# Optimization experiments

Measured on AMD Instinct MI355X. Metric: run time of the kernel, lower is better.

Reference implementation:

```python
import jax, jax.numpy as jnp
import numpy as np

B, S, D, H, MLP, RH, RANK, BS, E, RES = 64, 197, 768, 12, 3072, 512, 256, 2, 3, 1
EPS = 1e-5


def _ln(x, g, b):
    m = jnp.mean(x, -1, keepdims=True)
    v = jnp.mean((x - m) ** 2, -1, keepdims=True)
    return (x - m) / jnp.sqrt(v + EPS) * g + b


def setup_inputs() -> dict:
    key = jax.random.key(0)
    ks = jax.random.split(key, 16)
    n = lambda k, shp, s: (jax.random.normal(k, shp) * s).astype(jnp.float32)
    inp = {
        'x': n(ks[0], (B, S, D), 1.0),
        'LRA_mask': jnp.arange(2 ** BS, dtype=jnp.int32),
        'wq_w': n(ks[1], (D, D), 0.02), 'wq_b': jnp.zeros((D,), jnp.float32),
        'wk_w': n(ks[2], (D, D), 0.02), 'wk_b': jnp.zeros((D,), jnp.float32),
        'wv_w': n(ks[3], (D, D), 0.02), 'wv_b': jnp.zeros((D,), jnp.float32),
        'wo_w': n(ks[4], (D, D), 0.02), 'wo_b': jnp.zeros((D,), jnp.float32),
        'an_g': jnp.ones((D,), jnp.float32), 'an_b': jnp.zeros((D,), jnp.float32),
        'fc1_w': n(ks[5], (MLP, D), 0.02), 'fc1_b': jnp.zeros((MLP,), jnp.float32),
        'fc2_w': n(ks[6], (D, MLP), 0.02), 'fc2_b': jnp.zeros((D,), jnp.float32),
        'fn_g': jnp.ones((D,), jnp.float32), 'fn_b': jnp.zeros((D,), jnp.float32),
        'r1_w': n(ks[7], (RH, D), 0.01), 'r1_b': jnp.zeros((RH,), jnp.float32),
        'rn_g': jnp.ones((RH,), jnp.float32), 'rn_b': jnp.zeros((RH,), jnp.float32),
        'r2_w': n(ks[8], (BS * 2, RH), 0.01),
        'r2_b': jnp.array([0.1, 5.0] * BS, jnp.float32),
        'eA': n(ks[9], (E, RANK, D), 0.01),  # down_proj weights [out=rank, in=dim]
        'eB': n(ks[10], (E, D, RANK), 0.01),  # up_proj weights [out=dim, in=rank]
    }
    return inp


def reference(x, LRA_mask, wq_w, wq_b, wk_w, wk_b, wv_w, wv_b, wo_w, wo_b,
              an_g, an_b, fc1_w, fc1_b, fc2_w, fc2_b, fn_g, fn_b,
              r1_w, r1_b, rn_g, rn_b, r2_w, r2_b, eA, eB):
    hd = D // H
    # ---- RouterModule (eval mode: argmax hard routing) on block input ----
    rlog = jax.nn.silu(_ln(x @ r1_w.T + r1_b, rn_g, rn_b)) @ r2_w.T + r2_b
    rlog = rlog.reshape(B, S, BS, 2)
    bits = jnp.argmax(rlog, -1)               # [B,S,BS], value of channel-1 one-hot
    bits = bits.at[:, :RES, :].set(1)          # reserved tokens -> full-one key (identity)
    pw = 2 ** jnp.arange(BS - 1, -1, -1)
    idx = jnp.sum(bits * pw, -1)               # [B,S] routing key per token
    # ---- Attention (pre-norm) ----
    h = _ln(x, an_g, an_b)
    q = (h @ wq_w.T + wq_b).reshape(B, S, H, hd).transpose(0, 2, 1, 3)
    k = (h @ wk_w.T + wk_b).reshape(B, S, H, hd).transpose(0, 2, 1, 3)
    v = (h @ wv_w.T + wv_b).reshape(B, S, H, hd).transpose(0, 2, 1, 3)
    att = jax.nn.softmax(jnp.einsum('bhqd,bhkd->bhqk', q, k) / np.float32(np.sqrt(hd)), -1)
    o = jnp.einsum('bhqk,bhkd->bhqd', att, v).transpose(0, 2, 1, 3).reshape(B, S, D)
    x1 = x + (o @ wo_w.T + wo_b)
    # ---- FeedForward (pre-norm, exact GELU like torch nn.GELU) ----
    x2 = x1 + (jax.nn.gelu(_ln(x1, fn_g, fn_b) @ fc1_w.T + fc1_b, approximate=False) @ fc2_w.T + fc2_b)
    # ---- BlockPathApproximators: disjoint per-key residual LoRA experts ----
    # keys 0..E-1 have experts; key 2^BS-1 (full-one) is identity. LRA_mask covers all keys.
    down = jnp.einsum('bsd,erd->bser', x2, eA)            # [B,S,E,RANK]
    up = jnp.einsum('bser,edr->bsed', down, eB)           # [B,S,E,D]
    sel = (idx[..., None] == jnp.arange(E)).astype(x2.dtype)  # one-hot over experts [B,S,E]
    out = x2 + jnp.einsum('bsed,bse->bsd', up, sel)
    return out
```

## Files before the change

kernel.cpp:

```cpp
#include <hip/hip_runtime.h>
#include <cstdint>

#define B_SZ   64
#define SEQ    197
#define DIM    768
#define NHEAD  12
#define HDK    64
#define MLP_D  3072
#define RH_D   512
#define RANK_D 256
#define NEXP   3
#define TOK    (B_SZ*SEQ)

typedef unsigned short u16;
typedef __attribute__((ext_vector_type(8))) short s16x8;
typedef __attribute__((ext_vector_type(4))) float f32x4;

static __device__ __forceinline__ u16 f2bf(float f) {
  unsigned u = __builtin_bit_cast(unsigned, f);
  u = u + 0x7FFFu + ((u >> 16) & 1u);
  return (u16)(u >> 16);
}

static __device__ __forceinline__ f32x4 mfma16(s16x8 a, s16x8 b, f32x4 c) {
  return __builtin_amdgcn_mfma_f32_16x16x32_bf16(a, b, c, 0, 0, 0);
}

static __device__ __forceinline__ void gload16(const u16* g, u16* l) {
  __builtin_amdgcn_global_load_lds(
      (const __attribute__((address_space(1))) unsigned int*)(const void*)g,
      (__attribute__((address_space(3))) unsigned int*)(void*)l,
      16, 0, 0);
}

static __device__ __forceinline__ float gelu_fast(float v) {
  const float u2 = 2.f * v * (0.7978845608f + 0.0356774081f * v * v);
  return v / (1.f + __expf(-u2));
}

__global__ void cvt_bf16(const float* __restrict__ in, u16* __restrict__ out, long n) {
  long i = ((long)blockIdx.x * blockDim.x + threadIdx.x) * 4;
  const long stride = (long)gridDim.x * blockDim.x * 4;
  for (; i < n; i += stride) {
    float4 v = *(const float4*)(in + i);
    unsigned r0 = (unsigned)f2bf(v.x) | ((unsigned)f2bf(v.y) << 16);
    unsigned r1 = (unsigned)f2bf(v.z) | ((unsigned)f2bf(v.w) << 16);
    *(uint2*)(out + i) = make_uint2(r0, r1);
  }
}

__global__ void concat3(const float* __restrict__ a, const float* __restrict__ b,
                        const float* __restrict__ c, float* __restrict__ out) {
  int i = blockIdx.x * 256 + threadIdx.x;
  if (i < DIM) { out[i] = a[i]; out[DIM + i] = b[i]; out[2*DIM + i] = c[i]; }
}

__global__ __launch_bounds__(256) void ln_rows(
    const float* __restrict__ x, const float* __restrict__ g,
    const float* __restrict__ bb, u16* __restrict__ out, int M)
{
  const int row = blockIdx.x * 4 + (threadIdx.x >> 6);
  const int lane = threadIdx.x & 63;
  if (row >= M) return;
  const float* xr = x + (long)row * DIM;
  float4 v[3];
  float s = 0.f, s2 = 0.f;
#pragma unroll
  for (int c = 0; c < 3; ++c) {
    v[c] = *(const float4*)(xr + c*256 + lane*4);
    s  += v[c].x + v[c].y + v[c].z + v[c].w;
    s2 += v[c].x*v[c].x + v[c].y*v[c].y + v[c].z*v[c].z + v[c].w*v[c].w;
  }
#pragma unroll
  for (int o = 1; o < 64; o <<= 1) { s += __shfl_xor(s, o); s2 += __shfl_xor(s2, o); }
  const float mean = s * (1.f/DIM);
  const float var  = s2 * (1.f/DIM) - mean*mean;
  const float rstd = rsqrtf(fmaxf(var, 0.f) + 1e-5f);
#pragma unroll
  for (int c = 0; c < 3; ++c) {
    const int idx = c*256 + lane*4;
    float4 gg = *(const float4*)(g + idx);
    float4 be = *(const float4*)(bb + idx);
    float y0 = (v[c].x - mean)*rstd*gg.x + be.x;
    float y1 = (v[c].y - mean)*rstd*gg.y + be.y;
    float y2 = (v[c].z - mean)*rstd*gg.z + be.z;
    float y3 = (v[c].w - mean)*rstd*gg.w + be.w;
    unsigned r0 = (unsigned)f2bf(y0) | ((unsigned)f2bf(y1) << 16);
    unsigned r1 = (unsigned)f2bf(y2) | ((unsigned)f2bf(y3) << 16);
    *(uint2*)(out + (long)row*DIM + idx) = make_uint2(r0, r1);
  }
}

template<int ACT, bool HAS_RES, bool OUT_F32, bool OUT_BF16>
__global__ __launch_bounds__(256) void gemm_bt(
    const u16* __restrict__ A, const u16* __restrict__ Bm,
    const float* __restrict__ bias, const float* __restrict__ res,
    float* __restrict__ Cf, u16* __restrict__ Cb,
    int ldc, int M, int N, int K)
{
  __shared__ __align__(16) u16 lA[2][128*32];
  __shared__ __align__(16) u16 lB[2][128*32];
  const int tid  = threadIdx.x;
  const int lane = tid & 63;
  const int wave = tid >> 6;
  const int m0 = blockIdx.y * 128;
  const int n0 = blockIdx.x * 128;
  const int fr = lane & 15, fg = lane >> 4;
  const int wr = wave >> 1, wc = wave & 1;
  const int srow = tid >> 2;
  const int scol = (tid & 3) * 8;

  const int ra0 = (m0 + srow      < M) ? (m0 + srow)      : (M - 1);
  const int ra1 = (m0 + 64 + srow < M) ? (m0 + 64 + srow) : (M - 1);
  const u16* pa0 = A  + (long)ra0 * K + scol;
  const u16* pa1 = A  + (long)ra1 * K + scol;
  const u16* pb0 = Bm + (long)(n0 + srow) * K + scol;
  const u16* pb1 = Bm + (long)(n0 + 64 + srow) * K + scol;

  auto STAGE = [&](int buf, int kt) {
    gload16(pa0 + kt, &lA[buf][srow*32 + scol]);
    gload16(pa1 + kt, &lA[buf][(64 + srow)*32 + scol]);
    gload16(pb0 + kt, &lB[buf][srow*32 + scol]);
    gload16(pb1 + kt, &lB[buf][(64 + srow)*32 + scol]);
  };

  f32x4 acc[4][4] = {};

  STAGE(0, 0);
  __syncthreads();
  int cur = 0;
  const int nsteps = K >> 5;
  for (int t = 0; t < nsteps; ++t) {
    if (t + 1 < nsteps) STAGE(cur ^ 1, (t + 1) << 5);
    s16x8 af[4], bfr[4];
#pragma unroll
    for (int m = 0; m < 4; ++m) af[m]  = *(const s16x8*)&lA[cur][(wr*64 + m*16 + fr)*32 + fg*8];
#pragma unroll
    for (int n = 0; n < 4; ++n) bfr[n] = *(const s16x8*)&lB[cur][(wc*64 + n*16 + fr)*32 + fg*8];
#pragma unroll
    for (int m = 0; m < 4; ++m)
#pragma unroll
      for (int n = 0; n < 4; ++n)
        acc[m][n] = mfma16(af[m], bfr[n], acc[m][n]);
    __syncthreads();
    cur ^= 1;
  }

#pragma unroll
  for (int m = 0; m < 4; ++m) {
#pragma unroll
    for (int n = 0; n < 4; ++n) {
      const int col = n0 + wc*64 + n*16 + fr;
      const float bv = bias[col];
#pragma unroll
      for (int r = 0; r < 4; ++r) {
        const int row = m0 + wr*64 + m*16 + fg*4 + r;
        if (row < M) {
          float v = acc[m][n][r] + bv;
          if constexpr (ACT == 1) v = gelu_fast(v);
          if constexpr (HAS_RES) v += res[(long)row * N + col];
          if constexpr (OUT_F32) Cf[(long)row * ldc + col] = v;
          if constexpr (OUT_BF16) Cb[(long)row * ldc + col] = f2bf(v);
        }
      }
    }
  }
}

__global__ __launch_bounds__(256, 2) void attn(const u16* __restrict__ qkv, u16* __restrict__ o) {
  __shared__ __align__(16) u16 Vt[64][232];
  __shared__ __align__(16) u16 Pl[4][16][232];
  const int bh = blockIdx.x;
  const int b = bh / NHEAD, h = bh - b * NHEAD;
  const int tid = threadIdx.x, lane = tid & 63, wave = tid >> 6;
  const long rbase = (long)b * SEQ * 2304;

  for (int i = tid; i < 224*64; i += 256) {
    const int s = i >> 6, d = i & 63;
    u16 val = 0;
    if (s < SEQ) val = qkv[rbase + (long)s*2304 + 1536 + h*HDK + d];
    Vt[d][s] = val;
  }
  for (int i = lane; i < 16*24; i += 64) {
    Pl[wave][i / 24][208 + i % 24] = 0;
  }
  __syncthreads();

  const int fr = lane & 15, fg = lane >> 4;
  for (int qb = wave; qb < 13; qb += 4) {
    const int q0 = qb * 16;
    int qrow = q0 + fr; if (qrow > SEQ-1) qrow = SEQ-1;
    const u16* qp = qkv + rbase + (long)qrow*2304 + h*HDK;
    const s16x8 a0 = *(const s16x8*)(qp + fg*8);
    const s16x8 a1 = *(const s16x8*)(qp + 32 + fg*8);
    f32x4 sc[13];
    for (int kb = 0; kb < 13; ++kb) {
      int krow = kb*16 + fr; if (krow > SEQ-1) krow = SEQ-1;
      const u16* kp = qkv + rbase + (long)krow*2304 + DIM + h*HDK;
      const s16x8 b0 = *(const s16x8*)(kp + fg*8);
      const s16x8 b1 = *(const s16x8*)(kp + 32 + fg*8);
      f32x4 c = {0.f, 0.f, 0.f, 0.f};
      c = mfma16(a0, b0, c);
      c = mfma16(a1, b1, c);
      sc[kb] = c;
    }
    float inv[4];
#pragma unroll
    for (int r = 0; r < 4; ++r) {
      float mx = -3e38f;
      for (int kb = 0; kb < 13; ++kb) {
        const int col = kb*16 + fr;
        const float sv = sc[kb][r] * 0.125f;
        sc[kb][r] = sv;
        if (col < SEQ) mx = fmaxf(mx, sv);
      }
#pragma unroll
      for (int off = 1; off < 16; off <<= 1) mx = fmaxf(mx, __shfl_xor(mx, off));
      float sum = 0.f;
      for (int kb = 0; kb < 13; ++kb) {
        const int col = kb*16 + fr;
        const float p = (col < SEQ) ? __expf(sc[kb][r] - mx) : 0.f;
        sc[kb][r] = p;
        sum += p;
      }
#pragma unroll
      for (int off = 1; off < 16; off <<= 1) sum += __shfl_xor(sum, off);
      inv[r] = 1.f / sum;
    }
    asm volatile("s_waitcnt lgkmcnt(0)" ::: "memory");
    for (int kb = 0; kb < 13; ++kb) {
      const int col = kb*16 + fr;
#pragma unroll
      for (int r = 0; r < 4; ++r) Pl[wave][fg*4 + r][col] = f2bf(sc[kb][r]);
    }
    asm volatile("s_waitcnt lgkmcnt(0)" ::: "memory");
    for (int nb = 0; nb < 4; ++nb) {
      f32x4 acc = {0.f, 0.f, 0.f, 0.f};
#pragma unroll
      for (int kc = 0; kc < 7; ++kc) {
        const s16x8 pa = *(const s16x8*)&Pl[wave][fr][kc*32 + fg*8];
        const s16x8 vb = *(const s16x8*)&Vt[nb*16 + fr][kc*32 + fg*8];
        acc = mfma16(pa, vb, acc);
      }
#pragma unroll
      for (int r = 0; r < 4; ++r) {
        const int qr = q0 + fg*4 + r;
        if (qr < SEQ) o[((long)b*SEQ + qr)*DIM + h*HDK + nb*16 + fr] = f2bf(acc[r] * inv[r]);
      }
    }
  }
}

__global__ __launch_bounds__(64) void router_fin(
    const float* __restrict__ t1, const float* __restrict__ rg, const float* __restrict__ rb,
    const float* __restrict__ r2w, const float* __restrict__ r2b, int* __restrict__ idxb)
{
  const int t = blockIdx.x;
  const int lane = threadIdx.x;
  const float* row = t1 + (long)t * RH_D;
  float v[8];
  float s = 0.f, s2 = 0.f;
#pragma unroll
  for (int c = 0; c < 2; ++c) {
    float4 u = *(const float4*)(row + lane*8 + c*4);
    v[c*4+0]=u.x; v[c*4+1]=u.y; v[c*4+2]=u.z; v[c*4+3]=u.w;
    s += u.x+u.y+u.z+u.w;
    s2 += u.x*u.x+u.y*u.y+u.z*u.z+u.w*u.w;
  }
#pragma unroll
  for (int o = 1; o < 64; o <<= 1) { s += __shfl_xor(s, o); s2 += __shfl_xor(s2, o); }
  const float mean = s * (1.f/RH_D);
  const float var  = s2 * (1.f/RH_D) - mean*mean;
  const float rstd = rsqrtf(fmaxf(var, 0.f) + 1e-5f);
  float p[4] = {0.f, 0.f, 0.f, 0.f};
#pragma unroll
  for (int i = 0; i < 8; ++i) {
    const int col = lane*8 + i;
    float z = (v[i] - mean)*rstd*rg[col] + rb[col];
    z = z / (1.f + __expf(-z));
#pragma unroll
    for (int o = 0; o < 4; ++o) p[o] += z * r2w[o*RH_D + col];
  }
#pragma unroll
  for (int o = 0; o < 4; ++o)
#pragma unroll
    for (int off = 1; off < 64; off <<= 1) p[o] += __shfl_xor(p[o], off);
  if (lane == 0) {
    const float l0 = p[0]+r2b[0], l1 = p[1]+r2b[1], l2 = p[2]+r2b[2], l3 = p[3]+r2b[3];
    int b0 = (l1 > l0) ? 1 : 0;
    int b1 = (l3 > l2) ? 1 : 0;
    if (t % SEQ < 1) { b0 = 1; b1 = 1; }
    idxb[t] = b0*2 + b1;
  }
}

__global__ __launch_bounds__(256) void expert_apply(
    const int* __restrict__ idxb, const float* __restrict__ eA,
    const float* __restrict__ eB, float* __restrict__ out)
{
  const int t = blockIdx.x;
  const int e = idxb[t];
  if (e >= NEXP) return;
  __shared__ float xr[DIM];
  __shared__ float dn[RANK_D];
  const int tid = threadIdx.x;
  for (int i = tid; i < DIM; i += 256) xr[i] = out[(long)t*DIM + i];
  __syncthreads();
  {
    const float* ar = eA + ((long)e*RANK_D + tid)*DIM;
    float acc = 0.f;
    for (int k = 0; k < DIM; ++k) acc += ar[k]*xr[k];
    dn[tid] = acc;
  }
  __syncthreads();
  for (int d = tid; d < DIM; d += 256) {
    const float* br = eB + ((long)e*DIM + d)*RANK_D;
    float acc = 0.f;
    for (int r = 0; r < RANK_D; ++r) acc += br[r]*dn[r];
    out[(long)t*DIM + d] += acc;
  }
}

extern "C" void kernel_launch(void* const* d_in, const int* in_sizes, int n_in,
                              void* d_out, int out_size, void* d_ws, size_t ws_size,
                              hipStream_t stream) {
  (void)in_sizes; (void)n_in; (void)out_size;
  const float* x     = (const float*)d_in[0];
  const float* wq_w  = (const float*)d_in[2];
  const float* wq_b  = (const float*)d_in[3];
  const float* wk_w  = (const float*)d_in[4];
  const float* wk_b  = (const float*)d_in[5];
  const float* wv_w  = (const float*)d_in[6];
  const float* wv_b  = (const float*)d_in[7];
  const float* wo_w  = (const float*)d_in[8];
  const float* wo_b  = (const float*)d_in[9];
  const float* an_g  = (const float*)d_in[10];
  const float* an_b  = (const float*)d_in[11];
  const float* fc1_w = (const float*)d_in[12];
  const float* fc1_b = (const float*)d_in[13];
  const float* fc2_w = (const float*)d_in[14];
  const float* fc2_b = (const float*)d_in[15];
  const float* fn_g  = (const float*)d_in[16];
  const float* fn_b  = (const float*)d_in[17];
  const float* r1_w  = (const float*)d_in[18];
  const float* r1_b  = (const float*)d_in[19];
  const float* rn_g  = (const float*)d_in[20];
  const float* rn_b  = (const float*)d_in[21];
  const float* r2_w  = (const float*)d_in[22];
  const float* r2_b  = (const float*)d_in[23];
  const float* eA    = (const float*)d_in[24];
  const float* eB    = (const float*)d_in[25];
  float* outf = (float*)d_out;

  const size_t MiB = 1048576;
  const size_t NEED_FULL = 153*MiB;
  const size_t NEED_MIN  = 112*MiB + (size_t)TOK*DIM*2;
  if (ws_size < NEED_MIN) return;
  const bool full = (ws_size >= NEED_FULL);
  const int  nc   = full ? 1 : 2;
  const int  MC   = TOK / nc;
  const size_t offSY = full ? 94*MiB  : 72*MiB;
  const size_t offSZ = full ? 133*MiB : 112*MiB;

  char* ws = (char*)d_ws;
  u16*   Wqkv = (u16*)(ws + 0);
  u16*   Wo   = (u16*)(ws + 3538944);
  u16*   Wfc1 = (u16*)(ws + 4718592);
  u16*   Wfc2 = (u16*)(ws + 9437184);
  u16*   Wr1  = (u16*)(ws + 14155776);
  float* qkvb = (float*)(ws + 14942208);
  int*   idxb = (int*)(ws + 14952448);
  char* SX = ws + 16*MiB;
  char* SY = ws + offSY;
  char* SZ = ws + offSZ;
  u16*   x_b = (u16*)SX;
  u16*   qkv = (u16*)SX;
  u16*   m1  = (u16*)SX;
  float* t1  = (float*)SY;
  float* x1  = (float*)SY;
  u16*   h_b = (u16*)SZ;
  u16*   ob  = (u16*)SZ;
  u16*   h1  = (u16*)SZ;

  cvt_bf16<<<512, 256, 0, stream>>>(wq_w, Wqkv,               589824);
  cvt_bf16<<<512, 256, 0, stream>>>(wk_w, Wqkv + 589824,      589824);
  cvt_bf16<<<512, 256, 0, stream>>>(wv_w, Wqkv + 2*589824,    589824);
  cvt_bf16<<<512, 256, 0, stream>>>(wo_w, Wo,                 589824);
  cvt_bf16<<<1024, 256, 0, stream>>>(fc1_w, Wfc1,             2359296);
  cvt_bf16<<<1024, 256, 0, stream>>>(fc2_w, Wfc2,             2359296);
  cvt_bf16<<<512, 256, 0, stream>>>(r1_w, Wr1,                393216);
  cvt_bf16<<<2048, 256, 0, stream>>>(x, x_b,                  (long)TOK*DIM);
  concat3<<<3, 256, 0, stream>>>(wq_b, wk_b, wv_b, qkvb);

  gemm_bt<0, false, true, false><<<dim3(4, 99), 256, 0, stream>>>(
      x_b, Wr1, r1_b, nullptr, t1, nullptr, RH_D, TOK, RH_D, DIM);
  router_fin<<<TOK, 64, 0, stream>>>(t1, rn_g, rn_b, r2_w, r2_b, idxb);

  ln_rows<<<TOK/4, 256, 0, stream>>>(x, an_g, an_b, h_b, TOK);
  gemm_bt<0, false, false, true><<<dim3(18, 99), 256, 0, stream>>>(
      h_b, Wqkv, qkvb, nullptr, nullptr, qkv, 3*DIM, TOK, 3*DIM, DIM);
  attn<<<B_SZ*NHEAD, 256, 0, stream>>>(qkv, ob);
  gemm_bt<0, true, true, false><<<dim3(6, 99), 256, 0, stream>>>(
      ob, Wo, wo_b, x, x1, nullptr, DIM, TOK, DIM, DIM);

  ln_rows<<<TOK/4, 256, 0, stream>>>(x1, fn_g, fn_b, h1, TOK);
  for (int c = 0; c < nc; ++c) {
    const int r0 = c * MC;
    const int gy = (MC + 127) / 128;
    gemm_bt<1, false, false, true><<<dim3(24, gy), 256, 0, stream>>>(
        h1 + (long)r0*DIM, Wfc1, fc1_b, nullptr, nullptr, m1, MLP_D, MC, MLP_D, DIM);
    gemm_bt<0, true, true, false><<<dim3(6, gy), 256, 0, stream>>>(
        m1, Wfc2, fc2_b, x1 + (long)r0*DIM, outf + (long)r0*DIM, nullptr, DIM, MC, DIM, MLP_D);
  }

  expert_apply<<<TOK, 256, 0, stream>>>(idxb, eA, eB, outf);
}
```

Measured before the change: 512.4 us.

## Add 256x256-tile 8-wave GEMM kernel for QKV, out-proj and MLP GEMMs

Adds a new gemm8p kernel that computes 256x256 output tiles with 512 threads (8 waves), a compile-time K, double-buffered LDS fed by direct global-to-LDS loads, an XOR-swizzled layout, and setprio around the MFMA bursts. The QKV, output-projection, fc1 and fc2 GEMMs switch to it, while the router GEMM stays on the old kernel. Larger tiles raise arithmetic intensity per LDS and global load and cut the number of blocks. The costs are fewer blocks, so lower occupancy and possible tail effects (for example 150 blocks for the output projection), plus heavy register use from 32 accumulators per thread.

```diff
diff --git a/kernel.cpp b/kernel.cpp
--- a/kernel.cpp
+++ b/kernel.cpp
@@ -89,6 +89,112 @@
     unsigned r1 = (unsigned)f2bf(y2) | ((unsigned)f2bf(y3) << 16);
     *(uint2*)(out + (long)row*DIM + idx) = make_uint2(r0, r1);
   }
+}
+
+template<int ACT, bool HAS_RES, bool OUT_F32, bool OUT_BF16, int K>
+__global__ __launch_bounds__(512) void gemm8p(
+    const u16* __restrict__ A, const u16* __restrict__ Bm,
+    const float* __restrict__ bias, const float* __restrict__ res,
+    float* __restrict__ Cf, u16* __restrict__ Cb,
+    int ldc, int M, int N)
+{
+  __shared__ __align__(16) char lds2[2][32768];
+  const int tid  = threadIdx.x;
+  const int lane = tid & 63, wave = tid >> 6;
+  const int fr = lane & 15, fg = lane >> 4;
+  const int wr = wave >> 2, wcol = wave & 3;
+  const int m0 = blockIdx.y * 256, n0 = blockIdx.x * 256;
+
+  const int srow = tid >> 2;
+  const int g8 = (((tid & 3) ^ (srow & 3)) & 3) * 8;
+  const int ra_lo = (m0 + srow       < M) ? (m0 + srow)       : (M - 1);
+  const int ra_hi = (m0 + 128 + srow < M) ? (m0 + 128 + srow) : (M - 1);
+  const u16* pAlo = A  + (long)ra_lo * K + g8;
+  const u16* pAhi = A  + (long)ra_hi * K + g8;
+  const u16* pBlo = Bm + (long)(n0 + srow) * K + g8;
+  const u16* pBhi = Bm + (long)(n0 + 128 + srow) * K + g8;
+
+  const int abase = fr * 64 + (((fg ^ (fr & 3)) & 3) << 4);
+
+  auto STAGE4 = [&](int cb, int kt) {
+    char* d = &lds2[cb][0];
+    gload16(pAlo + kt, (u16*)(d)         + tid * 8);
+    gload16(pAhi + kt, (u16*)(d + 8192)  + tid * 8);
+    gload16(pBlo + kt, (u16*)(d + 16384) + tid * 8);
+    gload16(pBhi + kt, (u16*)(d + 24576) + tid * 8);
+  };
+
+  f32x4 acc[8][4] = {};
+
+  STAGE4(0, 0);
+  asm volatile("s_waitcnt vmcnt(0)" ::: "memory");
+  __builtin_amdgcn_s_barrier();
+
+  constexpr int NT = K / 32;
+  auto do_tile = [&](int t, char* bufc, int cnext) {
+    if (t + 1 < NT) STAGE4(cnext, (t + 1) * 32);
+    s16x8 a_[4], b_[4];
+#pragma unroll
+    for (int m = 0; m < 4; ++m)
+      a_[m] = *(const s16x8*)(bufc + wr*8192 + m*1024 + abase);
+#pragma unroll
+    for (int n = 0; n < 4; ++n)
+      b_[n] = *(const s16x8*)(bufc + 16384 + wcol*4096 + n*1024 + abase);
+    __builtin_amdgcn_s_barrier();
+    asm volatile("s_waitcnt lgkmcnt(0)" ::: "memory");
+    __builtin_amdgcn_sched_barrier(0);
+    __builtin_amdgcn_s_setprio(1);
+#pragma unroll
+    for (int m = 0; m < 4; ++m)
+#pragma unroll
+      for (int n = 0; n < 4; ++n)
+        acc[m][n] = mfma16(a_[m], b_[n], acc[m][n]);
+    __builtin_amdgcn_s_setprio(0);
+    __builtin_amdgcn_s_barrier();
+#pragma unroll
+    for (int m = 0; m < 4; ++m)
+      a_[m] = *(const s16x8*)(bufc + wr*8192 + 4096 + m*1024 + abase);
+    __builtin_amdgcn_s_barrier();
+    asm volatile("s_waitcnt lgkmcnt(0)" ::: "memory");
+    __builtin_amdgcn_sched_barrier(0);
+    __builtin_amdgcn_s_setprio(1);
+#pragma unroll
+    for (int m = 0; m < 4; ++m)
+#pragma unroll
+      for (int n = 0; n < 4; ++n)
+        acc[4 + m][n] = mfma16(a_[m], b_[n], acc[4 + m][n]);
+    __builtin_amdgcn_s_setprio(0);
+    asm volatile("s_waitcnt vmcnt(0)" ::: "memory");
+    __builtin_amdgcn_s_barrier();
+  };
+
+#pragma unroll 1
+  for (int t2 = 0; t2 < NT / 2; ++t2) {
+    do_tile(2 * t2,     &lds2[0][0], 1);
+    do_tile(2 * t2 + 1, &lds2[1][0], 0);
+  }
+
+#pragma unroll
+  for (int mh = 0; mh < 2; ++mh)
+#pragma unroll
+    for (int m = 0; m < 4; ++m)
+#pragma unroll
+      for (int n = 0; n < 4; ++n) {
+        const int col = n0 + wcol*64 + n*16 + fr;
+        const float bv = bias[col];
+        const int row0 = m0 + wr*128 + mh*64 + m*16 + fg*4;
+#pragma unroll
+        for (int rr = 0; rr < 4; ++rr) {
+          const int row = row0 + rr;
+          if (row < M) {
+            float v = acc[mh*4 + m][n][rr] + bv;
+            if constexpr (ACT == 1) v = gelu_fast(v);
+            if constexpr (HAS_RES) v += res[(long)row * N + col];
+            if constexpr (OUT_F32) Cf[(long)row * ldc + col] = v;
+            if constexpr (OUT_BF16) Cb[(long)row * ldc + col] = f2bf(v);
+          }
+        }
+      }
 }
 
 template<int ACT, bool HAS_RES, bool OUT_F32, bool OUT_BF16>
@@ -397,20 +503,20 @@
   router_fin<<<TOK, 64, 0, stream>>>(t1, rn_g, rn_b, r2_w, r2_b, idxb);
 
   ln_rows<<<TOK/4, 256, 0, stream>>>(x, an_g, an_b, h_b, TOK);
-  gemm_bt<0, false, false, true><<<dim3(18, 99), 256, 0, stream>>>(
-      h_b, Wqkv, qkvb, nullptr, nullptr, qkv, 3*DIM, TOK, 3*DIM, DIM);
+  gemm8p<0, false, false, true, DIM><<<dim3(9, 50), 512, 0, stream>>>(
+      h_b, Wqkv, qkvb, nullptr, nullptr, qkv, 3*DIM, TOK, 3*DIM);
   attn<<<B_SZ*NHEAD, 256, 0, stream>>>(qkv, ob);
-  gemm_bt<0, true, true, false><<<dim3(6, 99), 256, 0, stream>>>(
-      ob, Wo, wo_b, x, x1, nullptr, DIM, TOK, DIM, DIM);
+  gemm8p<0, true, true, false, DIM><<<dim3(3, 50), 512, 0, stream>>>(
+      ob, Wo, wo_b, x, x1, nullptr, DIM, TOK, DIM);
 
   ln_rows<<<TOK/4, 256, 0, stream>>>(x1, fn_g, fn_b, h1, TOK);
   for (int c = 0; c < nc; ++c) {
     const int r0 = c * MC;
-    const int gy = (MC + 127) / 128;
-    gemm_bt<1, false, false, true><<<dim3(24, gy), 256, 0, stream>>>(
-        h1 + (long)r0*DIM, Wfc1, fc1_b, nullptr, nullptr, m1, MLP_D, MC, MLP_D, DIM);
-    gemm_bt<0, true, true, false><<<dim3(6, gy), 256, 0, stream>>>(
-        m1, Wfc2, fc2_b, x1 + (long)r0*DIM, outf + (long)r0*DIM, nullptr, DIM, MC, DIM, MLP_D);
+    const int gy = (MC + 255) / 256;
+    gemm8p<1, false, false, true, DIM><<<dim3(12, gy), 512, 0, stream>>>(
+        h1 + (long)r0*DIM, Wfc1, fc1_b, nullptr, nullptr, m1, MLP_D, MC, MLP_D);
+    gemm8p<0, true, true, false, MLP_D><<<dim3(3, gy), 512, 0, stream>>>(
+        m1, Wfc2, fc2_b, x1 + (long)r0*DIM, outf + (long)r0*DIM, nullptr, DIM, MC, DIM);
   }
 
   expert_apply<<<TOK, 256, 0, stream>>>(idxb, eA, eB, outf);
```

Result: slower. 588.7 us (+14.9%).

## Triple-buffer GEMM LDS staging with XOR swizzle and explicit waitcnt pipelining

Applied to the files above, without the earlier changes.

Rewrites the shared bf16 GEMM main loop to use three LDS buffers with two tiles of prefetch in flight. A single barrier per step is placed after an explicit vmcnt wait, replacing the old syncthreads pair. LDS columns are XOR-swizzled to cut bank conflicts on fragment reads, and MFMA priority is raised with setprio. LDS use grows to 48KB per block with a 3-blocks-per-CU launch bound, and correctness depends on the hand-written waitcnt counts matching the async load behaviour.

```diff
diff --git a/kernel.cpp b/kernel.cpp
--- a/kernel.cpp
+++ b/kernel.cpp
@@ -92,14 +92,14 @@
 }
 
 template<int ACT, bool HAS_RES, bool OUT_F32, bool OUT_BF16>
-__global__ __launch_bounds__(256) void gemm_bt(
+__global__ __launch_bounds__(256, 3) void gemm_p3(
     const u16* __restrict__ A, const u16* __restrict__ Bm,
     const float* __restrict__ bias, const float* __restrict__ res,
     float* __restrict__ Cf, u16* __restrict__ Cb,
     int ldc, int M, int N, int K)
 {
-  __shared__ __align__(16) u16 lA[2][128*32];
-  __shared__ __align__(16) u16 lB[2][128*32];
+  __shared__ __align__(16) u16 lA[3][128*32];
+  __shared__ __align__(16) u16 lB[3][128*32];
   const int tid  = threadIdx.x;
   const int lane = tid & 63;
   const int wave = tid >> 6;
@@ -107,43 +107,56 @@
   const int n0 = blockIdx.x * 128;
   const int fr = lane & 15, fg = lane >> 4;
   const int wr = wave >> 1, wc = wave & 1;
-  const int srow = tid >> 2;
-  const int scol = (tid & 3) * 8;
-
-  const int ra0 = (m0 + srow      < M) ? (m0 + srow)      : (M - 1);
-  const int ra1 = (m0 + 64 + srow < M) ? (m0 + 64 + srow) : (M - 1);
-  const u16* pa0 = A  + (long)ra0 * K + scol;
-  const u16* pa1 = A  + (long)ra1 * K + scol;
+
+  const int srow  = tid >> 2;
+  const int scol  = (((tid & 3) ^ ((tid >> 3) & 3)) & 3) * 8;
+  const int r0a = m0 + srow, r1a = m0 + 64 + srow;
+  const u16* pa0 = A  + (long)((r0a < M) ? r0a : M - 1) * K + scol;
+  const u16* pa1 = A  + (long)((r1a < M) ? r1a : M - 1) * K + scol;
   const u16* pb0 = Bm + (long)(n0 + srow) * K + scol;
   const u16* pb1 = Bm + (long)(n0 + 64 + srow) * K + scol;
-
-  auto STAGE = [&](int buf, int kt) {
-    gload16(pa0 + kt, &lA[buf][srow*32 + scol]);
-    gload16(pa1 + kt, &lA[buf][(64 + srow)*32 + scol]);
-    gload16(pb0 + kt, &lB[buf][srow*32 + scol]);
-    gload16(pb1 + kt, &lB[buf][(64 + srow)*32 + scol]);
+  const int soff = tid * 8;
+
+  auto STAGE = [&](int b, int kt) {
+    gload16(pa0 + kt, &lA[b][soff]);
+    gload16(pa1 + kt, &lA[b][soff + 2048]);
+    gload16(pb0 + kt, &lB[b][soff]);
+    gload16(pb1 + kt, &lB[b][soff + 2048]);
   };
 
+  const int abase = fr * 32 + (((fg ^ (fr >> 1)) & 3) << 3);
+
   f32x4 acc[4][4] = {};
+  const int NT = K >> 5;
 
   STAGE(0, 0);
-  __syncthreads();
+  STAGE(1, 32);
+
   int cur = 0;
-  const int nsteps = K >> 5;
-  for (int t = 0; t < nsteps; ++t) {
-    if (t + 1 < nsteps) STAGE(cur ^ 1, (t + 1) << 5);
+#pragma unroll 1
+  for (int t = 0; t < NT; ++t) {
+    if (t < NT - 1) { asm volatile("s_waitcnt vmcnt(4)" ::: "memory"); }
+    else           { asm volatile("s_waitcnt vmcnt(0)" ::: "memory"); }
+    __builtin_amdgcn_s_barrier();
+    if (t + 2 < NT) {
+      int b2 = cur - 1; if (b2 < 0) b2 = 2;
+      STAGE(b2, (t + 2) << 5);
+    }
     s16x8 af[4], bfr[4];
 #pragma unroll
-    for (int m = 0; m < 4; ++m) af[m]  = *(const s16x8*)&lA[cur][(wr*64 + m*16 + fr)*32 + fg*8];
-#pragma unroll
-    for (int n = 0; n < 4; ++n) bfr[n] = *(const s16x8*)&lB[cur][(wc*64 + n*16 + fr)*32 + fg*8];
+    for (int m = 0; m < 4; ++m) af[m]  = *(const s16x8*)&lA[cur][wr*2048 + m*512 + abase];
+#pragma unroll
+    for (int n = 0; n < 4; ++n) bfr[n] = *(const s16x8*)&lB[cur][wc*2048 + n*512 + abase];
+    asm volatile("s_waitcnt lgkmcnt(0)" ::: "memory");
+    __builtin_amdgcn_sched_barrier(0);
+    __builtin_amdgcn_s_setprio(1);
 #pragma unroll
     for (int m = 0; m < 4; ++m)
 #pragma unroll
       for (int n = 0; n < 4; ++n)
         acc[m][n] = mfma16(af[m], bfr[n], acc[m][n]);
-    __syncthreads();
-    cur ^= 1;
+    __builtin_amdgcn_s_setprio(0);
+    cur = (cur == 2) ? 0 : cur + 1;
   }
 
 #pragma unroll
@@ -392,24 +405,24 @@
   cvt_bf16<<<2048, 256, 0, stream>>>(x, x_b,                  (long)TOK*DIM);
   concat3<<<3, 256, 0, stream>>>(wq_b, wk_b, wv_b, qkvb);
 
-  gemm_bt<0, false, true, false><<<dim3(4, 99), 256, 0, stream>>>(
+  gemm_p3<0, false, true, false><<<dim3(4, 99), 256, 0, stream>>>(
       x_b, Wr1, r1_b, nullptr, t1, nullptr, RH_D, TOK, RH_D, DIM);
   router_fin<<<TOK, 64, 0, stream>>>(t1, rn_g, rn_b, r2_w, r2_b, idxb);
 
   ln_rows<<<TOK/4, 256, 0, stream>>>(x, an_g, an_b, h_b, TOK);
-  gemm_bt<0, false, false, true><<<dim3(18, 99), 256, 0, stream>>>(
+  gemm_p3<0, false, false, true><<<dim3(18, 99), 256, 0, stream>>>(
       h_b, Wqkv, qkvb, nullptr, nullptr, qkv, 3*DIM, TOK, 3*DIM, DIM);
   attn<<<B_SZ*NHEAD, 256, 0, stream>>>(qkv, ob);
-  gemm_bt<0, true, true, false><<<dim3(6, 99), 256, 0, stream>>>(
+  gemm_p3<0, true, true, false><<<dim3(6, 99), 256, 0, stream>>>(
       ob, Wo, wo_b, x, x1, nullptr, DIM, TOK, DIM, DIM);
 
   ln_rows<<<TOK/4, 256, 0, stream>>>(x1, fn_g, fn_b, h1, TOK);
   for (int c = 0; c < nc; ++c) {
     const int r0 = c * MC;
     const int gy = (MC + 127) / 128;
-    gemm_bt<1, false, false, true><<<dim3(24, gy), 256, 0, stream>>>(
+    gemm_p3<1, false, false, true><<<dim3(24, gy), 256, 0, stream>>>(
         h1 + (long)r0*DIM, Wfc1, fc1_b, nullptr, nullptr, m1, MLP_D, MC, MLP_D, DIM);
-    gemm_bt<0, true, true, false><<<dim3(6, gy), 256, 0, stream>>>(
+    gemm_p3<0, true, true, false><<<dim3(6, gy), 256, 0, stream>>>(
         m1, Wfc2, fc2_b, x1 + (long)r0*DIM, outf + (long)r0*DIM, nullptr, DIM, MC, DIM, MLP_D);
   }
 
```

After: 536.6 us. 4.7% more time.
